# Kernel optimization log

Measured on AMD Instinct MI355X. Metric: run time of the kernel, lower is better.

The kernel has to match this reference:

```python
import jax, jax.numpy as jnp
import numpy as np

N_NODES = 50000
N_EDGES = 640000
N_REL = 200
D_IN = 128
D_OUT = 128


def setup_inputs() -> dict:
    key = jax.random.key(0)
    k1, k2, k3, k4, k5, k6 = jax.random.split(key, 6)
    x = jax.random.normal(k1, (N_NODES, D_IN), dtype=jnp.float32)
    edge_index = jax.random.randint(k2, (2, N_EDGES), 0, N_NODES, dtype=jnp.int64)
    edge_type = jax.random.randint(k3, (N_EDGES,), 0, N_REL, dtype=jnp.int64)
    rel_emb = jax.random.normal(k4, (N_REL, D_IN), dtype=jnp.float32)
    # nn.Linear weights stored as [out_features, in_features]
    W_lin = jax.random.normal(k5, (D_OUT, D_IN), dtype=jnp.float32) * (1.0 / np.sqrt(D_IN))
    # xavier_uniform for attn kernel [1, D_IN]
    limit = np.sqrt(6.0 / (1 + D_IN))
    W_attn = jax.random.uniform(k6, (1, D_IN), dtype=jnp.float32, minval=-limit, maxval=limit)
    return {"x": x, "edge_index": edge_index, "edge_type": edge_type,
            "rel_emb": rel_emb, "W_lin": W_lin, "W_attn": W_attn}


def reference(x, edge_index, edge_type, rel_emb, W_lin, W_attn):
    # x: [N, D_in]; edge_index: [2, E]; edge_type: [E]; rel_emb: [R, D_in]
    x_trans = x @ W_lin.T                       # [N, D_out]
    src_idx, tgt_idx = edge_index[0], edge_index[1]
    h_src = x[src_idx]                          # [E, D_in] gather
    h_rel = rel_emb[edge_type]                  # [E, D_in] gather
    sum_feat = h_src + h_rel                    # [E, D_in]
    attn = jax.nn.sigmoid(sum_feat @ W_attn.T)  # [E, 1]
    msg = x_trans[src_idx] * attn               # [E, D_out]
    out = jax.ops.segment_sum(msg, tgt_idx, num_segments=x.shape[0])  # [N, D_out]
    return jax.nn.relu(out)
```

## Files before the change

kernel.cpp:

```cpp
#include <hip/hip_runtime.h>
#include <hip/hip_bf16.h>

#define N_NODES 50000
#define N_EDGES 640000
#define N_REL   200
#define D       128
#define CAP     64
#define RANGES  8
#define NODES_PER_RANGE (N_NODES / RANGES)
#define CHUNK_EDGES 2560
#define N_CHUNKS (N_EDGES / CHUNK_EDGES)

#define XT_WAVES   (N_NODES / 16)
#define XT_BLOCKS  782
#define SREL_BLOCKS 50
#define CNT_BLOCKS 196
#define PRE_BLOCKS (XT_BLOCKS + SREL_BLOCKS + CNT_BLOCKS)

#define G_BLOCKS_PER_RANGE 391

typedef __attribute__((ext_vector_type(8))) short short8;
typedef __attribute__((ext_vector_type(4))) float floatx4;
typedef __attribute__((ext_vector_type(4))) unsigned uintx4;

__device__ __forceinline__ unsigned short f2bf(float f) {
    unsigned u = __float_as_uint(f);
    u += 0x7FFF + ((u >> 16) & 1);
    return (unsigned short)(u >> 16);
}

__device__ __forceinline__ float sigmoidf(float x) {
    return 1.f / (1.f + __expf(-x));
}

__global__ __launch_bounds__(256) void pre_kernel(
        const float* __restrict__ x,
        const float* __restrict__ W,
        const float* __restrict__ rel,
        const float* __restrict__ Wattn,
        unsigned short* __restrict__ xt,
        float* __restrict__ s_node,
        float* __restrict__ s_rel,
        int* __restrict__ count) {
    __shared__ unsigned short lw[D * D];
    const int b = blockIdx.x;

    if (b < XT_BLOCKS) {
        const int tid = threadIdx.x;
#pragma unroll
        for (int i = 0; i < 8; ++i) {
            const int idx8 = tid + i * 256;
            const int row  = idx8 >> 4;
            const int kk   = idx8 & 15;
            const float* __restrict__ wr = W + (size_t)row * D + kk * 8;
            const float4 lo = *(const float4*)(wr);
            const float4 hi = *(const float4*)(wr + 4);
            short8 v;
            v[0] = (short)f2bf(lo.x); v[1] = (short)f2bf(lo.y);
            v[2] = (short)f2bf(lo.z); v[3] = (short)f2bf(lo.w);
            v[4] = (short)f2bf(hi.x); v[5] = (short)f2bf(hi.y);
            v[6] = (short)f2bf(hi.z); v[7] = (short)f2bf(hi.w);
            const int slot = (row * 16 + kk) ^ (row & 7);
            *(short8*)((char*)lw + slot * 16) = v;
        }
        __syncthreads();

        const int wid = b * 4 + (threadIdx.x >> 6);
        if (wid >= XT_WAVES) return;
        const int lane = threadIdx.x & 63;
        const int r16  = lane & 15;
        const int quad = lane >> 4;
        const int m0   = wid * 16;

        short8 af[4];
        float  sn = 0.f;
#pragma unroll
        for (int s = 0; s < 4; ++s) {
            const int k0 = s * 32 + quad * 8;
            const float* __restrict__ xr = x + (size_t)(m0 + r16) * D + k0;
            const float4 lo = *(const float4*)(xr);
            const float4 hi = *(const float4*)(xr + 4);
            const float4 wl = *(const float4*)(Wattn + k0);
            const float4 wh = *(const float4*)(Wattn + k0 + 4);
            sn = fmaf(lo.x, wl.x, sn); sn = fmaf(lo.y, wl.y, sn);
            sn = fmaf(lo.z, wl.z, sn); sn = fmaf(lo.w, wl.w, sn);
            sn = fmaf(hi.x, wh.x, sn); sn = fmaf(hi.y, wh.y, sn);
            sn = fmaf(hi.z, wh.z, sn); sn = fmaf(hi.w, wh.w, sn);
            short8 a;
            a[0] = (short)f2bf(lo.x); a[1] = (short)f2bf(lo.y);
            a[2] = (short)f2bf(lo.z); a[3] = (short)f2bf(lo.w);
            a[4] = (short)f2bf(hi.x); a[5] = (short)f2bf(hi.y);
            a[6] = (short)f2bf(hi.z); a[7] = (short)f2bf(hi.w);
            af[s] = a;
        }
        sn += __shfl_xor(sn, 16);
        sn += __shfl_xor(sn, 32);
        if (lane < 16) s_node[m0 + r16] = sn;

#pragma unroll
        for (int t = 0; t < 8; ++t) {
            floatx4 acc = {0.f, 0.f, 0.f, 0.f};
            const int row = t * 16 + r16;
#pragma unroll
            for (int s = 0; s < 4; ++s) {
                const int slot = (row * 16 + s * 4 + quad) ^ (row & 7);
                const short8 bfrag = *(const short8*)((const char*)lw + slot * 16);
                acc = __builtin_amdgcn_mfma_f32_16x16x32_bf16(af[s], bfrag, acc, 0, 0, 0);
            }
#pragma unroll
            for (int r = 0; r < 4; ++r) {
                const int orow = m0 + quad * 4 + r;
                xt[(size_t)orow * D + t * 16 + r16] = f2bf(acc[r]);
            }
        }
    } else if (b < XT_BLOCKS + SREL_BLOCKS) {
        const int wave = (b - XT_BLOCKS) * 4 + (threadIdx.x >> 6);
        const int lane = threadIdx.x & 63;
        if (wave < N_REL) {
            const float* __restrict__ row = rel + (size_t)wave * D;
            float a = fmaf(row[lane], Wattn[lane],
                           row[lane + 64] * Wattn[lane + 64]);
#pragma unroll
            for (int off = 32; off; off >>= 1)
                a += __shfl_down(a, off);
            if (lane == 0) s_rel[wave] = a;
        }
    } else {
        const int i = (b - XT_BLOCKS - SREL_BLOCKS) * 256 + threadIdx.x;
        if (i < N_NODES) count[i] = 0;
    }
}

__global__ __launch_bounds__(256) void scatter_kernel(
        const int* __restrict__ src_idx,
        const int* __restrict__ tgt_idx,
        const int* __restrict__ etype,
        const float* __restrict__ s_node,
        const float* __restrict__ s_rel,
        int* __restrict__ count,
        unsigned* __restrict__ sorted) {
    __shared__ float ls_rel[N_REL];
    if (threadIdx.x < N_REL) ls_rel[threadIdx.x] = s_rel[threadIdx.x];
    __syncthreads();

    const int b     = blockIdx.x;
    const int lo    = (b & 7) * NODES_PER_RANGE;
    const int hi    = lo + NODES_PER_RANGE;
    const int base  = (b >> 3) * CHUNK_EDGES + threadIdx.x;

#pragma unroll
    for (int it = 0; it < CHUNK_EDGES / 256; ++it) {
        const int e = base + it * 256;
        const int t = tgt_idx[e];
        const int s = src_idx[e];
        const int r = etype[e];
        if (t >= lo && t < hi) {
            const float logit = s_node[s] + ls_rel[r];
            const unsigned rec =
                ((unsigned)f2bf(sigmoidf(logit)) << 16) | (unsigned)s;
            const int k = atomicAdd(&count[t], 1);
            sorted[t * CAP + k] = rec;
        }
    }
}

__device__ __forceinline__ void gproc4(unsigned r, const unsigned short* __restrict__ xt,
                                       int sub, floatx4& a0, floatx4& a1) {
    const unsigned src = r & 0xFFFFu;
    const float a = __uint_as_float(r & 0xFFFF0000u);
    const uint4 p = *(const uint4*)(xt + (size_t)src * D + sub * 8);
    a0[0] = fmaf(a, __uint_as_float(p.x << 16),         a0[0]);
    a0[1] = fmaf(a, __uint_as_float(p.x & 0xFFFF0000u), a0[1]);
    a0[2] = fmaf(a, __uint_as_float(p.y << 16),         a0[2]);
    a0[3] = fmaf(a, __uint_as_float(p.y & 0xFFFF0000u), a0[3]);
    a1[0] = fmaf(a, __uint_as_float(p.z << 16),         a1[0]);
    a1[1] = fmaf(a, __uint_as_float(p.z & 0xFFFF0000u), a1[1]);
    a1[2] = fmaf(a, __uint_as_float(p.w << 16),         a1[2]);
    a1[3] = fmaf(a, __uint_as_float(p.w & 0xFFFF0000u), a1[3]);
}

__global__ __launch_bounds__(256) void gather_kernel(
        const int* __restrict__ count,
        const unsigned* __restrict__ sorted,
        const unsigned short* __restrict__ xt,
        float* __restrict__ out) {
    const int rng   = blockIdx.x & 7;
    const int idx   = blockIdx.x >> 3;
    const int w     = threadIdx.x >> 6;
    const int lane  = threadIdx.x & 63;
    const int q     = lane >> 4;
    const int sub   = lane & 15;
    const int local = idx * 16 + w * 4 + q;
    if (local >= NODES_PER_RANGE) return;
    const int t = rng * NODES_PER_RANGE + local;

    const int cnt = count[t];
    const unsigned* __restrict__ rec = sorted + (size_t)t * CAP;

    floatx4 a0 = {0.f, 0.f, 0.f, 0.f};
    floatx4 a1 = {0.f, 0.f, 0.f, 0.f};
    int i = 0;
    for (; i + 4 <= cnt; i += 4) {
        const uintx4 r4 = __builtin_nontemporal_load((const uintx4*)(rec + i));
        gproc4(r4.x, xt, sub, a0, a1);
        gproc4(r4.y, xt, sub, a0, a1);
        gproc4(r4.z, xt, sub, a0, a1);
        gproc4(r4.w, xt, sub, a0, a1);
    }
    for (; i < cnt; ++i)
        gproc4(__builtin_nontemporal_load(rec + i), xt, sub, a0, a1);

    floatx4 o0, o1;
    o0[0] = fmaxf(a0[0], 0.f); o0[1] = fmaxf(a0[1], 0.f);
    o0[2] = fmaxf(a0[2], 0.f); o0[3] = fmaxf(a0[3], 0.f);
    o1[0] = fmaxf(a1[0], 0.f); o1[1] = fmaxf(a1[1], 0.f);
    o1[2] = fmaxf(a1[2], 0.f); o1[3] = fmaxf(a1[3], 0.f);
    floatx4* orow = (floatx4*)(out + (size_t)t * D) + sub * 2;
    __builtin_nontemporal_store(o0, orow);
    __builtin_nontemporal_store(o1, orow + 1);
}

extern "C" void kernel_launch(void* const* d_in, const int* in_sizes, int n_in,
                              void* d_out, int out_size, void* d_ws, size_t ws_size,
                              hipStream_t stream) {
    const float* x        = (const float*)d_in[0];
    const int*   edge_idx = (const int*)d_in[1];
    const int*   etype    = (const int*)d_in[2];
    const float* rel_emb  = (const float*)d_in[3];
    const float* W_lin    = (const float*)d_in[4];
    const float* W_attn   = (const float*)d_in[5];
    float* out = (float*)d_out;

    const int* src_idx = edge_idx;
    const int* tgt_idx = edge_idx + N_EDGES;

    unsigned short* xt   = (unsigned short*)d_ws;
    float* s_node        = (float*)(xt + (size_t)N_NODES * D);
    float* s_rel         = s_node + N_NODES;
    int*   count         = (int*)(s_rel + N_REL);
    unsigned* sorted     = (unsigned*)(count + N_NODES);

    pre_kernel<<<dim3(PRE_BLOCKS), dim3(256), 0, stream>>>(
        x, W_lin, rel_emb, W_attn, xt, s_node, s_rel, count);

    scatter_kernel<<<dim3(N_CHUNKS * RANGES), dim3(256), 0, stream>>>(
        src_idx, tgt_idx, etype, s_node, s_rel, count, sorted);

    gather_kernel<<<dim3(G_BLOCKS_PER_RANGE * RANGES), dim3(256), 0, stream>>>(
        count, sorted, xt, out);
}
```

Baseline: 155.5 us.

## Split s_node prep into own kernel and co-schedule xt GEMM with edge scatter

The attention dot product per node (s_node), s_rel and the count reset move into a small prep kernel. The bf16 GEMM producing xt and the edge scatter then share one launch, with block groups interleaved so the compute-heavy and atomic-heavy work can overlap. xt loads and stores also become nontemporal. The cost is an extra full read of x in the prep kernel, plus a larger shared-memory footprint for scatter blocks, which now allocate the 32KB weight tile too.

```diff
diff --git a/kernel.cpp b/kernel.cpp
--- a/kernel.cpp
+++ b/kernel.cpp
@@ -11,11 +11,16 @@
 #define CHUNK_EDGES 2560
 #define N_CHUNKS (N_EDGES / CHUNK_EDGES)
 
+#define SN_BLOCKS   6250
+#define SREL_BLOCKS 50
+#define CNT_BLOCKS  196
+#define PREP_BLOCKS (SN_BLOCKS + SREL_BLOCKS + CNT_BLOCKS)
+
 #define XT_WAVES   (N_NODES / 16)
 #define XT_BLOCKS  782
-#define SREL_BLOCKS 50
-#define CNT_BLOCKS 196
-#define PRE_BLOCKS (XT_BLOCKS + SREL_BLOCKS + CNT_BLOCKS)
+#define XT_GROUPS  98
+#define SC_GROUPS  N_CHUNKS
+#define TOT_GROUPS (XT_GROUPS + SC_GROUPS)
 
 #define G_BLOCKS_PER_RANGE 391
 
@@ -33,19 +38,64 @@
     return 1.f / (1.f + __expf(-x));
 }
 
-__global__ __launch_bounds__(256) void pre_kernel(
+__global__ __launch_bounds__(256) void prep_kernel(
         const float* __restrict__ x,
-        const float* __restrict__ W,
         const float* __restrict__ rel,
         const float* __restrict__ Wattn,
-        unsigned short* __restrict__ xt,
         float* __restrict__ s_node,
         float* __restrict__ s_rel,
         int* __restrict__ count) {
+    const int b = blockIdx.x;
+    if (b < SN_BLOCKS) {
+        const int node = b * 8 + (threadIdx.x >> 5);
+        const int sub  = threadIdx.x & 31;
+        if (node < N_NODES) {
+            const float4 xv = ((const float4*)(x + (size_t)node * D))[sub];
+            const float4 wv = ((const float4*)Wattn)[sub];
+            float a = xv.x * wv.x + xv.y * wv.y + xv.z * wv.z + xv.w * wv.w;
+#pragma unroll
+            for (int off = 16; off; off >>= 1)
+                a += __shfl_xor(a, off);
+            if (sub == 0) s_node[node] = a;
+        }
+    } else if (b < SN_BLOCKS + SREL_BLOCKS) {
+        const int wave = (b - SN_BLOCKS) * 4 + (threadIdx.x >> 6);
+        const int lane = threadIdx.x & 63;
+        if (wave < N_REL) {
+            const float* __restrict__ row = rel + (size_t)wave * D;
+            float a = fmaf(row[lane], Wattn[lane],
+                           row[lane + 64] * Wattn[lane + 64]);
+#pragma unroll
+            for (int off = 32; off; off >>= 1)
+                a += __shfl_down(a, off);
+            if (lane == 0) s_rel[wave] = a;
+        }
+    } else {
+        const int i = (b - SN_BLOCKS - SREL_BLOCKS) * 256 + threadIdx.x;
+        if (i < N_NODES) count[i] = 0;
+    }
+}
+
+__global__ __launch_bounds__(256) void fused_kernel(
+        const float* __restrict__ x,
+        const float* __restrict__ W,
+        unsigned short* __restrict__ xt,
+        const int* __restrict__ src_idx,
+        const int* __restrict__ tgt_idx,
+        const int* __restrict__ etype,
+        const float* __restrict__ s_node,
+        const float* __restrict__ s_rel,
+        int* __restrict__ count,
+        unsigned* __restrict__ sorted) {
     __shared__ unsigned short lw[D * D];
-    const int b = blockIdx.x;
-
-    if (b < XT_BLOCKS) {
+    __shared__ float ls_rel[N_REL];
+
+    const int g    = blockIdx.x >> 3;
+    const int sub8 = blockIdx.x & 7;
+    const int xg   = (g * XT_GROUPS) / TOT_GROUPS;
+    const bool is_x = (((g + 1) * XT_GROUPS) / TOT_GROUPS) > xg;
+
+    if (is_x) {
         const int tid = threadIdx.x;
 #pragma unroll
         for (int i = 0; i < 8; ++i) {
@@ -65,7 +115,7 @@
         }
         __syncthreads();
 
-        const int wid = b * 4 + (threadIdx.x >> 6);
+        const int wid = (xg * 8 + sub8) * 4 + (threadIdx.x >> 6);
         if (wid >= XT_WAVES) return;
         const int lane = threadIdx.x & 63;
         const int r16  = lane & 15;
@@ -73,29 +123,19 @@
         const int m0   = wid * 16;
 
         short8 af[4];
-        float  sn = 0.f;
 #pragma unroll
         for (int s = 0; s < 4; ++s) {
             const int k0 = s * 32 + quad * 8;
             const float* __restrict__ xr = x + (size_t)(m0 + r16) * D + k0;
-            const float4 lo = *(const float4*)(xr);
-            const float4 hi = *(const float4*)(xr + 4);
-            const float4 wl = *(const float4*)(Wattn + k0);
-            const float4 wh = *(const float4*)(Wattn + k0 + 4);
-            sn = fmaf(lo.x, wl.x, sn); sn = fmaf(lo.y, wl.y, sn);
-            sn = fmaf(lo.z, wl.z, sn); sn = fmaf(lo.w, wl.w, sn);
-            sn = fmaf(hi.x, wh.x, sn); sn = fmaf(hi.y, wh.y, sn);
-            sn = fmaf(hi.z, wh.z, sn); sn = fmaf(hi.w, wh.w, sn);
+            const floatx4 lo = __builtin_nontemporal_load((const floatx4*)(xr));
+            const floatx4 hi = __builtin_nontemporal_load((const floatx4*)(xr + 4));
             short8 a;
-            a[0] = (short)f2bf(lo.x); a[1] = (short)f2bf(lo.y);
-            a[2] = (short)f2bf(lo.z); a[3] = (short)f2bf(lo.w);
-            a[4] = (short)f2bf(hi.x); a[5] = (short)f2bf(hi.y);
-            a[6] = (short)f2bf(hi.z); a[7] = (short)f2bf(hi.w);
+            a[0] = (short)f2bf(lo[0]); a[1] = (short)f2bf(lo[1]);
+            a[2] = (short)f2bf(lo[2]); a[3] = (short)f2bf(lo[3]);
+            a[4] = (short)f2bf(hi[0]); a[5] = (short)f2bf(hi[1]);
+            a[6] = (short)f2bf(hi[2]); a[7] = (short)f2bf(hi[3]);
             af[s] = a;
         }
-        sn += __shfl_xor(sn, 16);
-        sn += __shfl_xor(sn, 32);
-        if (lane < 16) s_node[m0 + r16] = sn;
 
 #pragma unroll
         for (int t = 0; t < 8; ++t) {
@@ -110,56 +150,32 @@
 #pragma unroll
             for (int r = 0; r < 4; ++r) {
                 const int orow = m0 + quad * 4 + r;
-                xt[(size_t)orow * D + t * 16 + r16] = f2bf(acc[r]);
+                __builtin_nontemporal_store(f2bf(acc[r]),
+                    xt + (size_t)orow * D + t * 16 + r16);
             }
         }
-    } else if (b < XT_BLOCKS + SREL_BLOCKS) {
-        const int wave = (b - XT_BLOCKS) * 4 + (threadIdx.x >> 6);
-        const int lane = threadIdx.x & 63;
-        if (wave < N_REL) {
-            const float* __restrict__ row = rel + (size_t)wave * D;
-            float a = fmaf(row[lane], Wattn[lane],
-                           row[lane + 64] * Wattn[lane + 64]);
-#pragma unroll
-            for (int off = 32; off; off >>= 1)
-                a += __shfl_down(a, off);
-            if (lane == 0) s_rel[wave] = a;
-        }
     } else {
-        const int i = (b - XT_BLOCKS - SREL_BLOCKS) * 256 + threadIdx.x;
-        if (i < N_NODES) count[i] = 0;
-    }
-}
-
-__global__ __launch_bounds__(256) void scatter_kernel(
-        const int* __restrict__ src_idx,
-        const int* __restrict__ tgt_idx,
-        const int* __restrict__ etype,
-        const float* __restrict__ s_node,
-        const float* __restrict__ s_rel,
-        int* __restrict__ count,
-        unsigned* __restrict__ sorted) {
-    __shared__ float ls_rel[N_REL];
-    if (threadIdx.x < N_REL) ls_rel[threadIdx.x] = s_rel[threadIdx.x];
-    __syncthreads();
-
-    const int b     = blockIdx.x;
-    const int lo    = (b & 7) * NODES_PER_RANGE;
-    const int hi    = lo + NODES_PER_RANGE;
-    const int base  = (b >> 3) * CHUNK_EDGES + threadIdx.x;
-
-#pragma unroll
-    for (int it = 0; it < CHUNK_EDGES / 256; ++it) {
-        const int e = base + it * 256;
-        const int t = tgt_idx[e];
-        const int s = src_idx[e];
-        const int r = etype[e];
-        if (t >= lo && t < hi) {
-            const float logit = s_node[s] + ls_rel[r];
-            const unsigned rec =
-                ((unsigned)f2bf(sigmoidf(logit)) << 16) | (unsigned)s;
-            const int k = atomicAdd(&count[t], 1);
-            sorted[t * CAP + k] = rec;
+        if (threadIdx.x < N_REL) ls_rel[threadIdx.x] = s_rel[threadIdx.x];
+        __syncthreads();
+
+        const int sg   = g - xg;
+        const int lo   = sub8 * NODES_PER_RANGE;
+        const int hi   = lo + NODES_PER_RANGE;
+        const int base = sg * CHUNK_EDGES + threadIdx.x;
+
+#pragma unroll
+        for (int it = 0; it < CHUNK_EDGES / 256; ++it) {
+            const int e = base + it * 256;
+            const int t = tgt_idx[e];
+            const int s = src_idx[e];
+            const int r = etype[e];
+            if (t >= lo && t < hi) {
+                const float logit = s_node[s] + ls_rel[r];
+                const unsigned rec =
+                    ((unsigned)f2bf(sigmoidf(logit)) << 16) | (unsigned)s;
+                const int k = atomicAdd(&count[t], 1);
+                sorted[t * CAP + k] = rec;
+            }
         }
     }
 }
@@ -240,11 +256,11 @@
     int*   count         = (int*)(s_rel + N_REL);
     unsigned* sorted     = (unsigned*)(count + N_NODES);
 
-    pre_kernel<<<dim3(PRE_BLOCKS), dim3(256), 0, stream>>>(
-        x, W_lin, rel_emb, W_attn, xt, s_node, s_rel, count);
-
-    scatter_kernel<<<dim3(N_CHUNKS * RANGES), dim3(256), 0, stream>>>(
-        src_idx, tgt_idx, etype, s_node, s_rel, count, sorted);
+    prep_kernel<<<dim3(PREP_BLOCKS), dim3(256), 0, stream>>>(
+        x, rel_emb, W_attn, s_node, s_rel, count);
+
+    fused_kernel<<<dim3(TOT_GROUPS * 8), dim3(256), 0, stream>>>(
+        x, W_lin, xt, src_idx, tgt_idx, etype, s_node, s_rel, count, sorted);
 
     gather_kernel<<<dim3(G_BLOCKS_PER_RANGE * RANGES), dim3(256), 0, stream>>>(
         count, sorted, xt, out);
```

New measurement: 164.9 us. 1.06x slower.
